# Kernel optimization log

Hardware: AMD Instinct MI355X
Metric: run time of the kernel (lower is better)

Reference implementation:

```python
import jax, jax.numpy as jnp
import numpy as np

B, SQ, SK, D, DV = 16, 2048, 2048, 128, 128
NUM_HEADS = 2
DROPOUT_P = 0.1
SCALE_FACTOR = 1.0 / (DROPOUT_P * NUM_HEADS)  # = 5.0; scores are divided by this


def setup_inputs() -> dict:
    key = jax.random.key(0)
    k1, k2, k3, k4 = jax.random.split(key, 4)
    x1 = jax.random.normal(k1, (B, SQ, D), dtype=jnp.float32)
    x2 = jax.random.normal(k2, (B, SK, D), dtype=jnp.float32)
    x3 = jax.random.normal(k3, (B, SK, DV), dtype=jnp.float32)
    # deterministic dropout keep-mask (True -> keep), keep prob = 1 - p
    drop_mask = jax.random.bernoulli(k4, 1.0 - DROPOUT_P, (B, SQ, SK))
    return {"x1": x1, "x2": x2, "x3": x3, "drop_mask": drop_mask}


def reference(x1, x2, x3, drop_mask):
    # v1 = x1 @ x2^T : [B, Sq, Sk]
    scores = jnp.einsum("bqd,bkd->bqk", x1, x2)
    # v2 = v1 / scale_factor (scale_factor = 1/(p*heads) = 5 -> multiply by 0.2)
    scores = scores * (1.0 / SCALE_FACTOR)
    probs = jax.nn.softmax(scores, axis=-1)
    # dropout with inverted scaling 1/(1-p)
    keep_scale = 1.0 / (1.0 - DROPOUT_P)
    probs = jnp.where(drop_mask, probs * keep_scale, 0.0)
    # output = probs @ x3 : [B, Sq, Dv]
    return jnp.einsum("bqk,bkv->bqv", probs, x3)
```

## Files before the change

kernel.cpp:

```cpp
#include <hip/hip_runtime.h>
#include <stdint.h>


#define B_   16
#define SQ_  2048
#define SK_  2048
#define D_   128
#define DV_  128
#define BK   64
#define NT   (SK_ / BK)

typedef short  s16x8 __attribute__((ext_vector_type(8)));
typedef float  f32x4 __attribute__((ext_vector_type(4)));
typedef unsigned int u32x4 __attribute__((ext_vector_type(4)));
typedef unsigned short u16;
typedef unsigned int   u32;

__device__ __forceinline__ u32 pk2(float a, float b) {
    u32 r;
    asm("v_cvt_pk_bf16_f32 %0, %1, %2" : "=v"(r) : "v"(a), "v"(b));
    return r;
}
__device__ __forceinline__ u16 f2bf(float f) { return (u16)pk2(f, 0.0f); }

__device__ __forceinline__ void gload16(void* lds, const void* g) {
    __builtin_amdgcn_global_load_lds((const __attribute__((address_space(1))) u32*)g,
                                     (__attribute__((address_space(3))) u32*)lds,
                                     16, 0, 0);
}

__global__ __launch_bounds__(256)
void prep_k(const float* __restrict__ Kg, u16* __restrict__ Kz)
{
    int g   = blockIdx.x * 256 + threadIdx.x;
    int b   = g >> 15;
    int rem = g & 32767;
    int k   = rem >> 4;
    int grp = rem & 15;
    const float* src = Kg + ((size_t)b * SK_ + k) * D_ + grp * 8;
    float4 x = *(const float4*)(src);
    float4 y = *(const float4*)(src + 4);
    u32x4 w = { pk2(x.x, x.y), pk2(x.z, x.w), pk2(y.x, y.y), pk2(y.z, y.w) };
    int c = (grp * 8) ^ ((k & 7) << 3);
    *(u32x4*)(&Kz[((size_t)b * SK_ + k) * D_ + c]) = w;
}

__global__ __launch_bounds__(256)
void prep_v(const float* __restrict__ Vg, u16* __restrict__ Vz)
{
    int g  = blockIdx.x * 256 + threadIdx.x;
    int dv = g & 127;
    int kg = (g >> 7) & 7;
    int kt = (g >> 10) & 31;
    int b  = g >> 15;
    const float* src = Vg + ((size_t)b * SK_ + kt * 64 + kg * 8) * DV_ + dv;
    float v[8];
    #pragma unroll
    for (int jj = 0; jj < 8; ++jj) v[jj] = src[(size_t)jj * DV_];
    u32x4 w = { pk2(v[0], v[1]), pk2(v[2], v[3]), pk2(v[4], v[5]), pk2(v[6], v[7]) };
    int c = (kg * 8) ^ ((dv & 7) << 3);
    *(u32x4*)(&Vz[(((size_t)b * 32 + kt) * 128 + dv) * 64 + c]) = w;
}

#define STEP(IT, CUR, NXT, MC, MN)                                            \
  {                                                                           \
    if ((IT) + 1 < NT) {      \
      const u16* Kt = Kz + kvbase + (size_t)((IT) + 1) * 8192;                \
      const u16* Vt = Vz + kvbase + (size_t)((IT) + 1) * 8192;                \
      _Pragma("unroll")                                                       \
      for (int i = 0; i < 4; ++i) {                                           \
        int c16 = (wave * 4 + i) * 512;                                       \
        gload16(&Kbuf[NXT][c16], &Kt[c16 + lane * 8]);                        \
        gload16(&Vbuf[NXT][c16], &Vt[c16 + lane * 8]);                        \
      }                                                                       \
    }                                                                         \
    __builtin_amdgcn_sched_barrier(0);     \
    if ((IT) + 1 < NT) {   \
      _Pragma("unroll")                                                       \
      for (int qs = 0; qs < 2; ++qs)                                          \
        _Pragma("unroll")                                                     \
        for (int t = 0; t < 2; ++t)                                           \
          _Pragma("unroll")                                                   \
          for (int r = 0; r < 4; ++r)                                         \
            MN[qs][t][r] = mbase[(size_t)(qs * 16 + r) * SK_                  \
                                 + ((IT) + 1) * 64 + t * 16];                 \
    }                                                                         \
    f32x4 s[2][2];                                                            \
    _Pragma("unroll")                                                         \
    for (int qs = 0; qs < 2; ++qs)                                            \
      _Pragma("unroll")                                                       \
      for (int t = 0; t < 2; ++t) s[qs][t] = (f32x4){0.f, 0.f, 0.f, 0.f};     \
    __builtin_amdgcn_s_setprio(1);                                            \
    _Pragma("unroll")                                                         \
    for (int kb = 0; kb < 4; ++kb) {                                          \
      _Pragma("unroll")                                                       \
      for (int t = 0; t < 2; ++t) {                                           \
        int kcol = wk * 32 + t * 16 + n16;                                    \
        int coff = (kb * 32 + quad * 8) ^ ((kcol & 7) << 3);                  \
        s16x8 bK = *(const s16x8*)(&Kbuf[CUR][kcol * 128 + coff]);            \
        _Pragma("unroll")                                                     \
        for (int qs = 0; qs < 2; ++qs)                                        \
          s[qs][t] = __builtin_amdgcn_mfma_f32_16x16x32_bf16(aQ[qs][kb], bK,  \
                                                             s[qs][t], 0, 0, 0); \
      }                                                                       \
    }                                                                         \
    __builtin_amdgcn_s_setprio(0);                                            \
    _Pragma("unroll")                                                         \
    for (int qs = 0; qs < 2; ++qs)                                            \
      _Pragma("unroll")                                                       \
      for (int t = 0; t < 2; ++t)                                             \
        _Pragma("unroll")                                                     \
        for (int r = 0; r < 4; ++r) {                                         \
          float p = __builtin_amdgcn_exp2f(                                   \
              fmaf(s[qs][t][r], 0.28853901f, -17.3123405f));                  \
          l_part[qs][r] += p;                             \
          float pv = MC[qs][t][r] ? p : 0.f;                     \
          Ps[wave * 1280 + (qs * 16 + quad * 4 + r) * 40 + t * 16 + n16] = f2bf(pv); \
        }                                                                     \
    s16x8 aP0 = *(const s16x8*)(&Ps[wave * 1280 + n16 * 40 + quad * 8]);      \
    s16x8 aP1 = *(const s16x8*)(&Ps[wave * 1280 + (16 + n16) * 40 + quad * 8]); \
    __builtin_amdgcn_s_setprio(1);                                            \
    _Pragma("unroll")                                                         \
    for (int nt = 0; nt < 8; ++nt) {                                          \
      int dv = nt * 16 + n16;                                                 \
      int coff = (wk * 32 + quad * 8) ^ ((dv & 7) << 3);                      \
      s16x8 bV = *(const s16x8*)(&Vbuf[CUR][dv * 64 + coff]);                 \
      o[0][nt] = __builtin_amdgcn_mfma_f32_16x16x32_bf16(aP0, bV, o[0][nt], 0, 0, 0); \
      o[1][nt] = __builtin_amdgcn_mfma_f32_16x16x32_bf16(aP1, bV, o[1][nt], 0, 0, 0); \
    }                                                                         \
    __builtin_amdgcn_s_setprio(0);                                            \
         \
    asm volatile("s_waitcnt vmcnt(16)" ::: "memory");                         \
    __builtin_amdgcn_s_barrier();                                             \
    __builtin_amdgcn_sched_barrier(0);                                        \
  }

__global__ __launch_bounds__(256, 2)
void fattn_main(const float* __restrict__ Qg, const u16* __restrict__ Kz,
                const u16* __restrict__ Vz, const int* __restrict__ Mg,
                float* __restrict__ Og)
{
    __shared__ __align__(16) u16 Kbuf[2][64 * 128];
    __shared__ __align__(16) u16 Vbuf[2][128 * 64];
    __shared__ __align__(16) u16 Ps[4 * 32 * 40];
    __shared__ float lxch[64];

    const int tid  = threadIdx.x;
    const int wave = tid >> 6;
    const int lane = tid & 63;
    const int n16  = lane & 15;
    const int quad = lane >> 4;
    const int wq   = wave & 1;
    const int wk   = wave >> 1;

    const int raw = blockIdx.x;
    const int xcd = raw & 7;
    const int j   = raw >> 3;
    const int b   = xcd * 2 + (j & 1);
    const int qt  = j >> 1;
    const int q0  = qt << 6;

    s16x8 aQ[2][4];
    #pragma unroll
    for (int qs = 0; qs < 2; ++qs) {
        const float* qsrc = Qg + ((size_t)b * SQ_ + q0 + wq * 32 + qs * 16 + n16) * D_;
        #pragma unroll
        for (int kb = 0; kb < 4; ++kb) {
            float4 x = *(const float4*)(qsrc + kb * 32 + quad * 8);
            float4 y = *(const float4*)(qsrc + kb * 32 + quad * 8 + 4);
            u32x4 w = { pk2(x.x, x.y), pk2(x.z, x.w), pk2(y.x, y.y), pk2(y.z, y.w) };
            aQ[qs][kb] = __builtin_bit_cast(s16x8, w);
        }
    }

    f32x4 o[2][8];
    #pragma unroll
    for (int qs = 0; qs < 2; ++qs)
        #pragma unroll
        for (int i = 0; i < 8; ++i) o[qs][i] = (f32x4){0.f, 0.f, 0.f, 0.f};
    float l_part[2][4] = {{0.f, 0.f, 0.f, 0.f}, {0.f, 0.f, 0.f, 0.f}};

    const size_t kvbase = (size_t)b * 262144;

    const int* mbase = Mg + ((size_t)(b * SQ_ + q0 + wq * 32 + quad * 4)) * SK_
                     + wk * 32 + n16;

    {
        const u16* Kt = Kz + kvbase;
        const u16* Vt = Vz + kvbase;
        #pragma unroll
        for (int i = 0; i < 4; ++i) {
            int c16 = (wave * 4 + i) * 512;
            gload16(&Kbuf[0][c16], &Kt[c16 + lane * 8]);
            gload16(&Vbuf[0][c16], &Vt[c16 + lane * 8]);
        }
    }
    int mA[2][2][4], mB[2][2][4];
    #pragma unroll
    for (int qs = 0; qs < 2; ++qs)
        #pragma unroll
        for (int t = 0; t < 2; ++t)
            #pragma unroll
            for (int r = 0; r < 4; ++r)
                mA[qs][t][r] = mbase[(size_t)(qs * 16 + r) * SK_ + t * 16];

    __syncthreads();

    for (int it = 0; it < NT; it += 2) {
        STEP(it,     0, 1, mA, mB)
        STEP(it + 1, 1, 0, mB, mA)
    }

    float lr[2][4];
    #pragma unroll
    for (int qs = 0; qs < 2; ++qs)
        #pragma unroll
        for (int r = 0; r < 4; ++r) {
            float l = l_part[qs][r];
            #pragma unroll
            for (int off = 1; off < 16; off <<= 1) l += __shfl_xor(l, off);
            lr[qs][r] = l;
        }
    float* oxch = (float*)Kbuf;
    if (wk == 1) {
        #pragma unroll
        for (int qs = 0; qs < 2; ++qs)
            #pragma unroll
            for (int r = 0; r < 4; ++r) {
                int row = wq * 32 + qs * 16 + quad * 4 + r;
                #pragma unroll
                for (int nt = 0; nt < 8; ++nt)
                    oxch[row * 128 + nt * 16 + n16] = o[qs][nt][r];
                if (n16 == 0) lxch[row] = lr[qs][r];
            }
    }
    __syncthreads();
    if (wk == 0) {
        const float ksc = 1.0f / 0.9f;
        #pragma unroll
        for (int qs = 0; qs < 2; ++qs)
            #pragma unroll
            for (int r = 0; r < 4; ++r) {
                int row = wq * 32 + qs * 16 + quad * 4 + r;
                float inv = ksc / (lr[qs][r] + lxch[row]);
                size_t ob = ((size_t)b * SQ_ + q0 + row) * (size_t)DV_;
                #pragma unroll
                for (int nt = 0; nt < 8; ++nt)
                    Og[ob + nt * 16 + n16] =
                        (o[qs][nt][r] + oxch[row * 128 + nt * 16 + n16]) * inv;
            }
    }
}

#define BQ_FB 64
#define LDQ  136
#define LDK  136
#define LDVT 72
#define LDP  72

__global__ __launch_bounds__(256, 2)
void fattn_fb(const float* __restrict__ Qg, const float* __restrict__ Kg,
              const float* __restrict__ Vg, const int* __restrict__ Mg,
              float* __restrict__ Og)
{
    __shared__ u16 Qs[BQ_FB * LDQ];
    __shared__ u16 Ks[BK * LDK];
    __shared__ u16 Vt[DV_ * LDVT];
    __shared__ u16 Ps[4 * 16 * LDP];

    const int tid  = threadIdx.x;
    const int wave = tid >> 6;
    const int lane = tid & 63;
    const int n16  = lane & 15;
    const int quad = lane >> 4;

    const int raw = blockIdx.x;
    const int xcd = raw & 7;
    const int j   = raw >> 3;
    const int b   = xcd * 2 + (j & 1);
    const int q0  = (j >> 1) << 6;

    const int srow = tid >> 4;
    const int scol = (tid & 15) * 8;
    const int vrot = (tid & 7) * 8;

    {
        const float* src = Qg + ((size_t)b * SQ_ + q0) * D_;
        #pragma unroll
        for (int c = 0; c < 4; ++c) {
            int row = c * 16 + srow;
            float4 v0 = *(const float4*)(&src[row * D_ + scol]);
            float4 v1 = *(const float4*)(&src[row * D_ + scol + 4]);
            uint4 pk = { pk2(v0.x, v0.y), pk2(v0.z, v0.w),
                         pk2(v1.x, v1.y), pk2(v1.z, v1.w) };
            *(uint4*)(&Qs[row * LDQ + scol]) = pk;
        }
    }
    __syncthreads();

    s16x8 aQ[4];
    {
        const int qr = wave * 16 + n16;
        #pragma unroll
        for (int kb = 0; kb < 4; ++kb)
            aQ[kb] = *(const s16x8*)(&Qs[qr * LDQ + kb * 32 + quad * 8]);
    }

    f32x4 o[8];
    #pragma unroll
    for (int i = 0; i < 8; ++i) o[i] = (f32x4){0.f, 0.f, 0.f, 0.f};
    float l_part[4] = {0.f, 0.f, 0.f, 0.f};

    const size_t mask_qbase = ((size_t)b * SQ_ + q0 + wave * 16 + quad * 4) * (size_t)SK_;
    const float* baseK = Kg + ((size_t)b * SK_) * D_;
    const float* baseV = Vg + ((size_t)b * SK_) * DV_;

    float4 kf[8], vf[8];
    #pragma unroll
    for (int c = 0; c < 4; ++c) {
        int row = c * 16 + srow;
        kf[2*c]   = *(const float4*)(&baseK[row * D_ + scol]);
        kf[2*c+1] = *(const float4*)(&baseK[row * D_ + scol + 4]);
        vf[2*c]   = *(const float4*)(&baseV[row * DV_ + scol]);
        vf[2*c+1] = *(const float4*)(&baseV[row * DV_ + scol + 4]);
    }
    int mkc[4][4], mkn[4][4];
    #pragma unroll
    for (int t = 0; t < 4; ++t)
        #pragma unroll
        for (int r = 0; r < 4; ++r)
            mkc[t][r] = Mg[mask_qbase + (size_t)r * SK_ + (t * 16 + n16)];

    for (int it = 0; it < NT; ++it) {
        __syncthreads();
        #pragma unroll
        for (int c = 0; c < 4; ++c) {
            int row = c * 16 + srow;
            uint4 pk = { pk2(kf[2*c].x, kf[2*c].y),     pk2(kf[2*c].z, kf[2*c].w),
                         pk2(kf[2*c+1].x, kf[2*c+1].y), pk2(kf[2*c+1].z, kf[2*c+1].w) };
            *(uint4*)(&Ks[row * LDK + scol]) = pk;
        }
        #pragma unroll
        for (int c = 0; c < 4; ++c) {
            int k    = c * 16 + srow;
            int rcol = (k + vrot) & 63;
            int dv0  = scol;
            u32 r0 = pk2(vf[2*c].x,   vf[2*c].y);
            u32 r1 = pk2(vf[2*c].z,   vf[2*c].w);
            u32 r2 = pk2(vf[2*c+1].x, vf[2*c+1].y);
            u32 r3 = pk2(vf[2*c+1].z, vf[2*c+1].w);
            Vt[(dv0 + 0) * LDVT + rcol] = (u16)r0;
            Vt[(dv0 + 1) * LDVT + rcol] = (u16)(r0 >> 16);
            Vt[(dv0 + 2) * LDVT + rcol] = (u16)r1;
            Vt[(dv0 + 3) * LDVT + rcol] = (u16)(r1 >> 16);
            Vt[(dv0 + 4) * LDVT + rcol] = (u16)r2;
            Vt[(dv0 + 5) * LDVT + rcol] = (u16)(r2 >> 16);
            Vt[(dv0 + 6) * LDVT + rcol] = (u16)r3;
            Vt[(dv0 + 7) * LDVT + rcol] = (u16)(r3 >> 16);
        }
        if (it + 1 < NT) {
            const int k0n = (it + 1) * BK;
            #pragma unroll
            for (int c = 0; c < 4; ++c) {
                int row = k0n + c * 16 + srow;
                kf[2*c]   = *(const float4*)(&baseK[row * D_ + scol]);
                kf[2*c+1] = *(const float4*)(&baseK[row * D_ + scol + 4]);
                vf[2*c]   = *(const float4*)(&baseV[row * DV_ + scol]);
                vf[2*c+1] = *(const float4*)(&baseV[row * DV_ + scol + 4]);
            }
            #pragma unroll
            for (int t = 0; t < 4; ++t)
                #pragma unroll
                for (int r = 0; r < 4; ++r)
                    mkn[t][r] = Mg[mask_qbase + (size_t)r * SK_ + (k0n + t * 16 + n16)];
        }
        __syncthreads();

        f32x4 s[4];
        #pragma unroll
        for (int t = 0; t < 4; ++t) s[t] = (f32x4){0.f, 0.f, 0.f, 0.f};
        #pragma unroll
        for (int kb = 0; kb < 4; ++kb) {
            #pragma unroll
            for (int t = 0; t < 4; ++t) {
                s16x8 bK = *(const s16x8*)(&Ks[(t * 16 + n16) * LDK + kb * 32 + quad * 8]);
                s[t] = __builtin_amdgcn_mfma_f32_16x16x32_bf16(aQ[kb], bK, s[t], 0, 0, 0);
            }
        }
        #pragma unroll
        for (int t = 0; t < 4; ++t)
            #pragma unroll
            for (int r = 0; r < 4; ++r) {
                float p = __expf(fmaf(s[t][r], 0.2f, -12.0f));
                l_part[r] += p;
                float pv = mkc[t][r] ? p : 0.f;
                Ps[(wave * 16 + quad * 4 + r) * LDP + t * 16 + n16] = f2bf(pv);
            }
        #pragma unroll
        for (int kk = 0; kk < 2; ++kk) {
            s16x8 aP = *(const s16x8*)(&Ps[(wave * 16 + n16) * LDP + kk * 32 + quad * 8]);
            #pragma unroll
            for (int nt = 0; nt < 8; ++nt) {
                int dv   = nt * 16 + n16;
                int rcol = (kk * 32 + quad * 8 + 8 * ((dv >> 3) & 7)) & 63;
                s16x8 bV = *(const s16x8*)(&Vt[dv * LDVT + rcol]);
                o[nt] = __builtin_amdgcn_mfma_f32_16x16x32_bf16(aP, bV, o[nt], 0, 0, 0);
            }
        }
        #pragma unroll
        for (int t = 0; t < 4; ++t)
            #pragma unroll
            for (int r = 0; r < 4; ++r) mkc[t][r] = mkn[t][r];
    }

    const float keep_scale = 1.0f / 0.9f;
    #pragma unroll
    for (int r = 0; r < 4; ++r) {
        float l = l_part[r];
        #pragma unroll
        for (int off = 1; off < 16; off <<= 1)
            l += __shfl_xor(l, off);
        float inv_l = keep_scale / l;
        size_t obase = ((size_t)b * SQ_ + q0 + wave * 16 + quad * 4 + r) * DV_;
        #pragma unroll
        for (int nt = 0; nt < 8; ++nt)
            Og[obase + nt * 16 + n16] = o[nt][r] * inv_l;
    }
}

extern "C" void kernel_launch(void* const* d_in, const int* in_sizes, int n_in,
                              void* d_out, int out_size, void* d_ws, size_t ws_size,
                              hipStream_t stream) {
    const float* Qg = (const float*)d_in[0];
    const float* Kg = (const float*)d_in[1];
    const float* Vg = (const float*)d_in[2];
    const int*   Mg = (const int*)d_in[3];
    float* Og = (float*)d_out;
    if (d_ws != nullptr && ws_size >= (size_t)16 * 1024 * 1024) {
        u16* Kz = (u16*)d_ws;
        u16* Vz = Kz + 4194304;
        prep_k<<<dim3(2048), 256, 0, stream>>>(Kg, Kz);
        prep_v<<<dim3(2048), 256, 0, stream>>>(Vg, Vz);
        fattn_main<<<dim3(512), 256, 0, stream>>>(Qg, Kz, Vz, Mg, Og);
    } else {
        fattn_fb<<<dim3(512), 256, 0, stream>>>(Qg, Kg, Vg, Mg, Og);
    }
}
```

Measured before the change: 418.7 us.

## Load K and V fragments directly into registers, drop LDS staging and barriers

Replaces the double-buffered LDS staging of K and V (global_load_lds plus per-step waitcnt and block barrier) with direct per-lane global loads into MFMA operand registers. K for the next tile is prefetched into a register double buffer, and V for the current tile is loaded at the start of each step. The dropout mask is packed into a bitmask, and shared memory shrinks to a union of the P scratch and the epilogue exchange buffers. This removes block-wide barriers and LDS traffic, at the cost of more VGPRs, redundant global/L2 reads across waves, and V-load latency that sits on the critical path.

```diff
diff --git a/kernel.cpp b/kernel.cpp
--- a/kernel.cpp
+++ b/kernel.cpp
@@ -22,12 +22,6 @@
     return r;
 }
 __device__ __forceinline__ u16 f2bf(float f) { return (u16)pk2(f, 0.0f); }
-
-__device__ __forceinline__ void gload16(void* lds, const void* g) {
-    __builtin_amdgcn_global_load_lds((const __attribute__((address_space(1))) u32*)g,
-                                     (__attribute__((address_space(3))) u32*)lds,
-                                     16, 0, 0);
-}
 
 __global__ __launch_bounds__(256)
 void prep_k(const float* __restrict__ Kg, u16* __restrict__ Kz)
@@ -62,88 +56,92 @@
     *(u32x4*)(&Vz[(((size_t)b * 32 + kt) * 128 + dv) * 64 + c]) = w;
 }
 
-#define STEP(IT, CUR, NXT, MC, MN)                                            \
+#define STEP(IT, KC, KN)                                                      \
   {                                                                           \
-    if ((IT) + 1 < NT) {      \
-      const u16* Kt = Kz + kvbase + (size_t)((IT) + 1) * 8192;                \
-      const u16* Vt = Vz + kvbase + (size_t)((IT) + 1) * 8192;                \
-      _Pragma("unroll")                                                       \
-      for (int i = 0; i < 4; ++i) {                                           \
-        int c16 = (wave * 4 + i) * 512;                                       \
-        gload16(&Kbuf[NXT][c16], &Kt[c16 + lane * 8]);                        \
-        gload16(&Vbuf[NXT][c16], &Vt[c16 + lane * 8]);                        \
-      }                                                                       \
-    }                                                                         \
-    __builtin_amdgcn_sched_barrier(0);     \
-    if ((IT) + 1 < NT) {   \
+            \
+    u32 mcur = 0;                                                             \
+    _Pragma("unroll")                                                         \
+    for (int i = 0; i < 16; ++i)                                              \
+      mcur |= (mld[i] != 0 ? 1u : 0u) << i;                                   \
+               \
+    if ((IT) + 1 < NT) {                                                      \
       _Pragma("unroll")                                                       \
       for (int qs = 0; qs < 2; ++qs)                                          \
         _Pragma("unroll")                                                     \
         for (int t = 0; t < 2; ++t)                                           \
           _Pragma("unroll")                                                   \
           for (int r = 0; r < 4; ++r)                                         \
-            MN[qs][t][r] = mbase[(size_t)(qs * 16 + r) * SK_                  \
-                                 + ((IT) + 1) * 64 + t * 16];                 \
+            mld[qs * 8 + t * 4 + r] =                                         \
+                mbase[(size_t)(qs * 16 + r) * SK_ + ((IT) + 1) * 64 + t * 16];\
     }                                                                         \
-    f32x4 s[2][2];                                                            \
+          \
+    s16x8 vc[8];                                                              \
     _Pragma("unroll")                                                         \
-    for (int qs = 0; qs < 2; ++qs)                                            \
+    for (int nt = 0; nt < 8; ++nt)                                            \
+      vc[nt] = *(const s16x8*)(&Vz[kvbase + (size_t)(IT) * 8192               \
+                                   + (nt * 16 + n16) * 64 + vcoff]);          \
+                                 \
+    if ((IT) + 1 < NT) {                                                      \
       _Pragma("unroll")                                                       \
-      for (int t = 0; t < 2; ++t) s[qs][t] = (f32x4){0.f, 0.f, 0.f, 0.f};     \
-    __builtin_amdgcn_s_setprio(1);                                            \
+      for (int t = 0; t < 2; ++t)                                             \
+        _Pragma("unroll")                                                     \
+        for (int kb = 0; kb < 4; ++kb)                                        \
+          KN[t * 4 + kb] = *(const s16x8*)(                                   \
+              &Kz[kvbase + (size_t)((IT) + 1) * 8192                          \
+                  + (wk * 32 + t * 16 + n16) * 128                            \
+                  + ((kb * 32 + quad * 8) ^ kxor)]);                          \
+    }                                                                         \
+                      \
     _Pragma("unroll")                                                         \
-    for (int kb = 0; kb < 4; ++kb) {                                          \
+    for (int qs = 0; qs < 2; ++qs) {                                          \
+      f32x4 s0 = (f32x4){0.f, 0.f, 0.f, 0.f};                                 \
+      f32x4 s1 = (f32x4){0.f, 0.f, 0.f, 0.f};                                 \
+      __builtin_amdgcn_s_setprio(1);                                          \
       _Pragma("unroll")                                                       \
-      for (int t = 0; t < 2; ++t) {                                           \
-        int kcol = wk * 32 + t * 16 + n16;                                    \
-        int coff = (kb * 32 + quad * 8) ^ ((kcol & 7) << 3);                  \
-        s16x8 bK = *(const s16x8*)(&Kbuf[CUR][kcol * 128 + coff]);            \
-        _Pragma("unroll")                                                     \
-        for (int qs = 0; qs < 2; ++qs)                                        \
-          s[qs][t] = __builtin_amdgcn_mfma_f32_16x16x32_bf16(aQ[qs][kb], bK,  \
-                                                             s[qs][t], 0, 0, 0); \
+      for (int kb = 0; kb < 4; ++kb) {                                        \
+        s0 = __builtin_amdgcn_mfma_f32_16x16x32_bf16(aQ[qs][kb], KC[kb],      \
+                                                     s0, 0, 0, 0);            \
+        s1 = __builtin_amdgcn_mfma_f32_16x16x32_bf16(aQ[qs][kb], KC[4 + kb],  \
+                                                     s1, 0, 0, 0);            \
       }                                                                       \
-    }                                                                         \
-    __builtin_amdgcn_s_setprio(0);                                            \
-    _Pragma("unroll")                                                         \
-    for (int qs = 0; qs < 2; ++qs)                                            \
+      __builtin_amdgcn_s_setprio(0);                                          \
       _Pragma("unroll")                                                       \
       for (int t = 0; t < 2; ++t)                                             \
         _Pragma("unroll")                                                     \
         for (int r = 0; r < 4; ++r) {                                         \
+          float sv = t ? s1[r] : s0[r];                                       \
           float p = __builtin_amdgcn_exp2f(                                   \
-              fmaf(s[qs][t][r], 0.28853901f, -17.3123405f));                  \
+              fmaf(sv, 0.28853901f, -17.3123405f));                           \
           l_part[qs][r] += p;                             \
-          float pv = MC[qs][t][r] ? p : 0.f;                     \
-          Ps[wave * 1280 + (qs * 16 + quad * 4 + r) * 40 + t * 16 + n16] = f2bf(pv); \
+          float pv = ((mcur >> (qs * 8 + t * 4 + r)) & 1u) ? p : 0.f;         \
+          sh.Ps[wave * 1280 + (qs * 16 + quad * 4 + r) * 40 + t * 16 + n16] = \
+              f2bf(pv);                                                       \
         }                                                                     \
-    s16x8 aP0 = *(const s16x8*)(&Ps[wave * 1280 + n16 * 40 + quad * 8]);      \
-    s16x8 aP1 = *(const s16x8*)(&Ps[wave * 1280 + (16 + n16) * 40 + quad * 8]); \
+    }                                                                         \
+    s16x8 aP0 = *(const s16x8*)(&sh.Ps[wave * 1280 + n16 * 40 + quad * 8]);   \
+    s16x8 aP1 = *(const s16x8*)(&sh.Ps[wave * 1280 + (16 + n16) * 40 + quad * 8]); \
     __builtin_amdgcn_s_setprio(1);                                            \
     _Pragma("unroll")                                                         \
     for (int nt = 0; nt < 8; ++nt) {                                          \
-      int dv = nt * 16 + n16;                                                 \
-      int coff = (wk * 32 + quad * 8) ^ ((dv & 7) << 3);                      \
-      s16x8 bV = *(const s16x8*)(&Vbuf[CUR][dv * 64 + coff]);                 \
-      o[0][nt] = __builtin_amdgcn_mfma_f32_16x16x32_bf16(aP0, bV, o[0][nt], 0, 0, 0); \
-      o[1][nt] = __builtin_amdgcn_mfma_f32_16x16x32_bf16(aP1, bV, o[1][nt], 0, 0, 0); \
+      o[0][nt] = __builtin_amdgcn_mfma_f32_16x16x32_bf16(aP0, vc[nt],         \
+                                                         o[0][nt], 0, 0, 0);  \
+      o[1][nt] = __builtin_amdgcn_mfma_f32_16x16x32_bf16(aP1, vc[nt],         \
+                                                         o[1][nt], 0, 0, 0);  \
     }                                                                         \
     __builtin_amdgcn_s_setprio(0);                                            \
-         \
-    asm volatile("s_waitcnt vmcnt(16)" ::: "memory");                         \
-    __builtin_amdgcn_s_barrier();                                             \
-    __builtin_amdgcn_sched_barrier(0);                                        \
   }
+
+union ShMem {
+    u16 Ps[4 * 32 * 40];
+    struct { float oxch[64 * 128]; float lxch[64]; } ep;
+};
 
 __global__ __launch_bounds__(256, 2)
 void fattn_main(const float* __restrict__ Qg, const u16* __restrict__ Kz,
                 const u16* __restrict__ Vz, const int* __restrict__ Mg,
                 float* __restrict__ Og)
 {
-    __shared__ __align__(16) u16 Kbuf[2][64 * 128];
-    __shared__ __align__(16) u16 Vbuf[2][128 * 64];
-    __shared__ __align__(16) u16 Ps[4 * 32 * 40];
-    __shared__ float lxch[64];
+    __shared__ __align__(16) ShMem sh;
 
     const int tid  = threadIdx.x;
     const int wave = tid >> 6;
@@ -160,6 +158,9 @@
     const int qt  = j >> 1;
     const int q0  = qt << 6;
 
+    const int kxor  = (n16 & 7) << 3;
+    const int vcoff = (wk * 32 + quad * 8) ^ kxor;
+
     s16x8 aQ[2][4];
     #pragma unroll
     for (int qs = 0; qs < 2; ++qs) {
@@ -181,34 +182,29 @@
     float l_part[2][4] = {{0.f, 0.f, 0.f, 0.f}, {0.f, 0.f, 0.f, 0.f}};
 
     const size_t kvbase = (size_t)b * 262144;
-
     const int* mbase = Mg + ((size_t)(b * SQ_ + q0 + wq * 32 + quad * 4)) * SK_
                      + wk * 32 + n16;
 
-    {
-        const u16* Kt = Kz + kvbase;
-        const u16* Vt = Vz + kvbase;
-        #pragma unroll
-        for (int i = 0; i < 4; ++i) {
-            int c16 = (wave * 4 + i) * 512;
-            gload16(&Kbuf[0][c16], &Kt[c16 + lane * 8]);
-            gload16(&Vbuf[0][c16], &Vt[c16 + lane * 8]);
-        }
-    }
-    int mA[2][2][4], mB[2][2][4];
+    s16x8 k0[8], k1[8];
+    #pragma unroll
+    for (int t = 0; t < 2; ++t)
+        #pragma unroll
+        for (int kb = 0; kb < 4; ++kb)
+            k0[t * 4 + kb] = *(const s16x8*)(
+                &Kz[kvbase + (wk * 32 + t * 16 + n16) * 128
+                    + ((kb * 32 + quad * 8) ^ kxor)]);
+    int mld[16];
     #pragma unroll
     for (int qs = 0; qs < 2; ++qs)
         #pragma unroll
         for (int t = 0; t < 2; ++t)
             #pragma unroll
             for (int r = 0; r < 4; ++r)
-                mA[qs][t][r] = mbase[(size_t)(qs * 16 + r) * SK_ + t * 16];
-
-    __syncthreads();
+                mld[qs * 8 + t * 4 + r] = mbase[(size_t)(qs * 16 + r) * SK_ + t * 16];
 
     for (int it = 0; it < NT; it += 2) {
-        STEP(it,     0, 1, mA, mB)
-        STEP(it + 1, 1, 0, mB, mA)
+        STEP(it,     k0, k1)
+        STEP(it + 1, k1, k0)
     }
 
     float lr[2][4];
@@ -221,7 +217,7 @@
             for (int off = 1; off < 16; off <<= 1) l += __shfl_xor(l, off);
             lr[qs][r] = l;
         }
-    float* oxch = (float*)Kbuf;
+    __syncthreads();
     if (wk == 1) {
         #pragma unroll
         for (int qs = 0; qs < 2; ++qs)
@@ -230,8 +226,8 @@
                 int row = wq * 32 + qs * 16 + quad * 4 + r;
                 #pragma unroll
                 for (int nt = 0; nt < 8; ++nt)
-                    oxch[row * 128 + nt * 16 + n16] = o[qs][nt][r];
-                if (n16 == 0) lxch[row] = lr[qs][r];
+                    sh.ep.oxch[row * 128 + nt * 16 + n16] = o[qs][nt][r];
+                if (n16 == 0) sh.ep.lxch[row] = lr[qs][r];
             }
     }
     __syncthreads();
@@ -242,12 +238,12 @@
             #pragma unroll
             for (int r = 0; r < 4; ++r) {
                 int row = wq * 32 + qs * 16 + quad * 4 + r;
-                float inv = ksc / (lr[qs][r] + lxch[row]);
+                float inv = ksc / (lr[qs][r] + sh.ep.lxch[row]);
                 size_t ob = ((size_t)b * SQ_ + q0 + row) * (size_t)DV_;
                 #pragma unroll
                 for (int nt = 0; nt < 8; ++nt)
                     Og[ob + nt * 16 + n16] =
-                        (o[qs][nt][r] + oxch[row * 128 + nt * 16 + n16]) * inv;
+                        (o[qs][nt][r] + sh.ep.oxch[row * 128 + nt * 16 + n16]) * inv;
             }
     }
 }
```

Measured after the change: 770.3 us. 1.84x slower.

## Load K tiles directly into registers and bit-pack dropout mask

Applied to the files above, without the earlier changes.

K fragments are now loaded straight from global memory into registers, double-buffered across iterations, instead of staged through shared memory. This removes the K LDS buffer and its LDS reads. The dropout mask is loaded with nontemporal loads and packed into a 16-bit register mask. The hand-tuned vmcnt wait plus barrier is replaced by a plain __syncthreads. The trade-off is higher register pressure and uncoalesced per-lane global K loads, and the full sync may serialize the pipeline more.

```diff
diff --git a/kernel.cpp b/kernel.cpp
--- a/kernel.cpp
+++ b/kernel.cpp
@@ -62,28 +62,39 @@
     *(u32x4*)(&Vz[(((size_t)b * 32 + kt) * 128 + dv) * 64 + c]) = w;
 }
 
-#define STEP(IT, CUR, NXT, MC, MN)                                            \
+#define STEP(IT, CUR, NXT, KC, KN)                                            \
   {                                                                           \
-    if ((IT) + 1 < NT) {      \
-      const u16* Kt = Kz + kvbase + (size_t)((IT) + 1) * 8192;                \
+            \
+    u32 mcur = 0;                                                             \
+    _Pragma("unroll")                                                         \
+    for (int i = 0; i < 16; ++i)                                              \
+      mcur |= (mld[i] != 0 ? 1u : 0u) << i;                                   \
+    if ((IT) + 1 < NT) {                                                      \
+                                       \
       const u16* Vt = Vz + kvbase + (size_t)((IT) + 1) * 8192;                \
       _Pragma("unroll")                                                       \
       for (int i = 0; i < 4; ++i) {                                           \
         int c16 = (wave * 4 + i) * 512;                                       \
-        gload16(&Kbuf[NXT][c16], &Kt[c16 + lane * 8]);                        \
         gload16(&Vbuf[NXT][c16], &Vt[c16 + lane * 8]);                        \
       }                                                                       \
-    }                                                                         \
-    __builtin_amdgcn_sched_barrier(0);     \
-    if ((IT) + 1 < NT) {   \
+              \
+      _Pragma("unroll")                                                       \
+      for (int t = 0; t < 2; ++t)                                             \
+        _Pragma("unroll")                                                     \
+        for (int kb = 0; kb < 4; ++kb)                                        \
+          KN[t * 4 + kb] = *(const s16x8*)(                                   \
+              &Kz[kvbase + (size_t)((IT) + 1) * 8192                          \
+                  + (wk * 32 + t * 16 + n16) * 128                            \
+                  + ((kb * 32 + quad * 8) ^ kxor)]);                          \
+             \
       _Pragma("unroll")                                                       \
       for (int qs = 0; qs < 2; ++qs)                                          \
         _Pragma("unroll")                                                     \
         for (int t = 0; t < 2; ++t)                                           \
           _Pragma("unroll")                                                   \
           for (int r = 0; r < 4; ++r)                                         \
-            MN[qs][t][r] = mbase[(size_t)(qs * 16 + r) * SK_                  \
-                                 + ((IT) + 1) * 64 + t * 16];                 \
+            mld[qs * 8 + t * 4 + r] = __builtin_nontemporal_load(             \
+                &mbase[(size_t)(qs * 16 + r) * SK_ + ((IT) + 1) * 64 + t * 16]); \
     }                                                                         \
     f32x4 s[2][2];                                                            \
     _Pragma("unroll")                                                         \
@@ -95,13 +106,10 @@
     for (int kb = 0; kb < 4; ++kb) {                                          \
       _Pragma("unroll")                                                       \
       for (int t = 0; t < 2; ++t) {                                           \
-        int kcol = wk * 32 + t * 16 + n16;                                    \
-        int coff = (kb * 32 + quad * 8) ^ ((kcol & 7) << 3);                  \
-        s16x8 bK = *(const s16x8*)(&Kbuf[CUR][kcol * 128 + coff]);            \
         _Pragma("unroll")                                                     \
         for (int qs = 0; qs < 2; ++qs)                                        \
-          s[qs][t] = __builtin_amdgcn_mfma_f32_16x16x32_bf16(aQ[qs][kb], bK,  \
-                                                             s[qs][t], 0, 0, 0); \
+          s[qs][t] = __builtin_amdgcn_mfma_f32_16x16x32_bf16(                 \
+              aQ[qs][kb], KC[t * 4 + kb], s[qs][t], 0, 0, 0);                 \
       }                                                                       \
     }                                                                         \
     __builtin_amdgcn_s_setprio(0);                                            \
@@ -114,25 +122,21 @@
           float p = __builtin_amdgcn_exp2f(                                   \
               fmaf(s[qs][t][r], 0.28853901f, -17.3123405f));                  \
           l_part[qs][r] += p;                             \
-          float pv = MC[qs][t][r] ? p : 0.f;                     \
-          Ps[wave * 1280 + (qs * 16 + quad * 4 + r) * 40 + t * 16 + n16] = f2bf(pv); \
+          float pv = ((mcur >> (qs * 8 + t * 4 + r)) & 1u) ? p : 0.f;         \
+          Ps[wave * 1280 + (qs * 16 + quad * 4 + r) * 40 + t * 16 + n16] =    \
+              f2bf(pv);                                                       \
         }                                                                     \
     s16x8 aP0 = *(const s16x8*)(&Ps[wave * 1280 + n16 * 40 + quad * 8]);      \
     s16x8 aP1 = *(const s16x8*)(&Ps[wave * 1280 + (16 + n16) * 40 + quad * 8]); \
     __builtin_amdgcn_s_setprio(1);                                            \
     _Pragma("unroll")                                                         \
     for (int nt = 0; nt < 8; ++nt) {                                          \
-      int dv = nt * 16 + n16;                                                 \
-      int coff = (wk * 32 + quad * 8) ^ ((dv & 7) << 3);                      \
-      s16x8 bV = *(const s16x8*)(&Vbuf[CUR][dv * 64 + coff]);                 \
+      s16x8 bV = *(const s16x8*)(&Vbuf[CUR][(nt * 16 + n16) * 64 + vcoff]);   \
       o[0][nt] = __builtin_amdgcn_mfma_f32_16x16x32_bf16(aP0, bV, o[0][nt], 0, 0, 0); \
       o[1][nt] = __builtin_amdgcn_mfma_f32_16x16x32_bf16(aP1, bV, o[1][nt], 0, 0, 0); \
     }                                                                         \
     __builtin_amdgcn_s_setprio(0);                                            \
-         \
-    asm volatile("s_waitcnt vmcnt(16)" ::: "memory");                         \
-    __builtin_amdgcn_s_barrier();                                             \
-    __builtin_amdgcn_sched_barrier(0);                                        \
+    __syncthreads();    \
   }
 
 __global__ __launch_bounds__(256, 2)
@@ -140,7 +144,6 @@
                 const u16* __restrict__ Vz, const int* __restrict__ Mg,
                 float* __restrict__ Og)
 {
-    __shared__ __align__(16) u16 Kbuf[2][64 * 128];
     __shared__ __align__(16) u16 Vbuf[2][128 * 64];
     __shared__ __align__(16) u16 Ps[4 * 32 * 40];
     __shared__ float lxch[64];
@@ -160,6 +163,9 @@
     const int qt  = j >> 1;
     const int q0  = qt << 6;
 
+    const int kxor  = (n16 & 7) << 3;
+    const int vcoff = (wk * 32 + quad * 8) ^ kxor;
+
     s16x8 aQ[2][4];
     #pragma unroll
     for (int qs = 0; qs < 2; ++qs) {
@@ -181,34 +187,40 @@
     float l_part[2][4] = {{0.f, 0.f, 0.f, 0.f}, {0.f, 0.f, 0.f, 0.f}};
 
     const size_t kvbase = (size_t)b * 262144;
-
     const int* mbase = Mg + ((size_t)(b * SQ_ + q0 + wq * 32 + quad * 4)) * SK_
                      + wk * 32 + n16;
 
     {
-        const u16* Kt = Kz + kvbase;
         const u16* Vt = Vz + kvbase;
         #pragma unroll
         for (int i = 0; i < 4; ++i) {
             int c16 = (wave * 4 + i) * 512;
-            gload16(&Kbuf[0][c16], &Kt[c16 + lane * 8]);
             gload16(&Vbuf[0][c16], &Vt[c16 + lane * 8]);
         }
     }
-    int mA[2][2][4], mB[2][2][4];
+    s16x8 k0[8], k1[8];
+    #pragma unroll
+    for (int t = 0; t < 2; ++t)
+        #pragma unroll
+        for (int kb = 0; kb < 4; ++kb)
+            k0[t * 4 + kb] = *(const s16x8*)(
+                &Kz[kvbase + (wk * 32 + t * 16 + n16) * 128
+                    + ((kb * 32 + quad * 8) ^ kxor)]);
+    int mld[16];
     #pragma unroll
     for (int qs = 0; qs < 2; ++qs)
         #pragma unroll
         for (int t = 0; t < 2; ++t)
             #pragma unroll
             for (int r = 0; r < 4; ++r)
-                mA[qs][t][r] = mbase[(size_t)(qs * 16 + r) * SK_ + t * 16];
+                mld[qs * 8 + t * 4 + r] = __builtin_nontemporal_load(
+                    &mbase[(size_t)(qs * 16 + r) * SK_ + t * 16]);
 
     __syncthreads();
 
     for (int it = 0; it < NT; it += 2) {
-        STEP(it,     0, 1, mA, mB)
-        STEP(it + 1, 1, 0, mB, mA)
+        STEP(it,     0, 1, k0, k1)
+        STEP(it + 1, 1, 0, k1, k0)
     }
 
     float lr[2][4];
@@ -221,7 +233,7 @@
             for (int off = 1; off < 16; off <<= 1) l += __shfl_xor(l, off);
             lr[qs][r] = l;
         }
-    float* oxch = (float*)Kbuf;
+    float* oxch = (float*)Vbuf;
     if (wk == 1) {
         #pragma unroll
         for (int qs = 0; qs < 2; ++qs)
```

Result: slower. 481.3 us (+14.9%).
